# Performance work log

Measured on AMD Instinct MI355X. Metric: run time of the kernel, lower is better.

## Reference

```python
import jax, jax.numpy as jnp
import numpy as np

WS = (4, 4, 4)          # window size (D, H, W)
DIM = 96
HEADS = 8
HEAD_DIM = DIM // HEADS
SCALE = HEAD_DIM ** (-0.5)
N = WS[0] * WS[1] * WS[2]  # 64 tokens per window


def _relative_position_index(ws):
    coords = np.stack(np.meshgrid(np.arange(ws[0]), np.arange(ws[1]), np.arange(ws[2]), indexing='ij'))
    cf = coords.reshape(3, -1)                       # [3, N]
    rel = cf[:, :, None] - cf[:, None, :]            # [3, N, N]
    rel = rel.transpose(1, 2, 0).astype(np.int64)    # [N, N, 3]
    rel[:, :, 0] += ws[0] - 1
    rel[:, :, 1] += ws[1] - 1
    rel[:, :, 2] += ws[2] - 1
    rel[:, :, 0] *= (2 * ws[1] - 1) * (2 * ws[2] - 1)
    rel[:, :, 1] *= 2 * ws[2] - 1
    return jnp.asarray(rel.sum(-1))                  # [N, N]

REL_IDX = _relative_position_index(WS)


def setup_inputs() -> dict:
    key = jax.random.key(0)
    ks = jax.random.split(key, 6)
    B = 4096   # total windows (64 images x 64 windows)
    nW = 64
    table_size = (2 * WS[0] - 1) * (2 * WS[1] - 1) * (2 * WS[2] - 1)  # 343
    return {
        'x': jax.random.normal(ks[0], (B, N, DIM), jnp.float32),
        'mask': jax.random.normal(ks[1], (nW, N, N), jnp.float32),
        'qkv_w': jax.random.normal(ks[2], (3 * DIM, DIM), jnp.float32) * 0.02,
        'proj_w': jax.random.normal(ks[3], (DIM, DIM), jnp.float32) * 0.02,
        'proj_b': jnp.zeros((DIM,), jnp.float32),
        'bias_table': jax.random.normal(ks[4], (table_size, HEADS), jnp.float32) * 0.02,
    }


def reference(x, mask, qkv_w, proj_w, proj_b, bias_table):
    B, n, C = x.shape
    # QKV projection (torch Linear: y = x @ W.T), split into heads
    qkv = (x @ qkv_w.T).reshape(B, n, 3, HEADS, HEAD_DIM)
    qkv = jnp.transpose(qkv, (2, 0, 3, 1, 4))        # [3, B, H, N, hd]
    q, k, v = qkv[0], qkv[1], qkv[2]
    attn = jnp.einsum('bhnd,bhmd->bhnm', q, k) * SCALE
    # gathered relative position bias: [N, N, H] -> [H, N, N]
    bias = bias_table[REL_IDX[:n, :n].reshape(-1)].reshape(n, n, HEADS)
    attn = attn + jnp.transpose(bias, (2, 0, 1))[None]
    # shifted-window mask add
    nW = mask.shape[0]
    attn = attn.reshape(B // nW, nW, HEADS, n, n) + mask[None, :, None]
    attn = attn.reshape(B, HEADS, n, n)
    attn = jax.nn.softmax(attn, axis=-1)
    out = jnp.einsum('bhnm,bhmd->bnhd', attn, v).reshape(B, n, C)
    return out @ proj_w.T + proj_b
```

## Files before the change

kernel.cpp:

```cpp
#include <hip/hip_runtime.h>
#include <hip/hip_bf16.h>
#include <stdint.h>


typedef float  f32x4  __attribute__((ext_vector_type(4)));
typedef float  f32x16 __attribute__((ext_vector_type(16)));
typedef short  short8 __attribute__((ext_vector_type(8)));

#define WS_WQKV_OFF   (8388608)
#define WS_WPROJT_OFF (8388608 + 55296)
#define LOG2E 1.4426950408889634f

__device__ __forceinline__ unsigned short f2bf(float f) {
  __hip_bfloat16 h = __float2bfloat16(f);
  return *reinterpret_cast<unsigned short*>(&h);
}
__device__ __forceinline__ uint32_t pack2(float a, float b) {
  __hip_bfloat162 h = __float22bfloat162_rn(float2{a, b});
  return *reinterpret_cast<uint32_t*>(&h);
}

__global__ void prep_weights(const float* __restrict__ qkv_w,
                             const float* __restrict__ proj_w,
                             unsigned short* __restrict__ ws16) {
  int tid = blockIdx.x * 256 + threadIdx.x;
  if (tid < 27648) {
    float v = qkv_w[tid];
    if (tid < 9216) v *= (0.28867513459481288f * LOG2E);
    ws16[WS_WQKV_OFF / 2 + tid] = f2bf(v);
  } else {
    int t = tid - 27648;
    int h = t / 1536, rem = t - h * 1536;
    int o = rem >> 4, c = rem & 15;
    float v = (c < 12) ? proj_w[o * 96 + h * 12 + c] : 0.f;
    ws16[WS_WPROJT_OFF / 2 + t] = f2bf(v);
  }
}

__global__ void prep_biasm(const float* __restrict__ mask,
                           const float* __restrict__ bias_table,
                           float* __restrict__ biasm) {
  int tid = blockIdx.x * 256 + threadIdx.x;
  int m = tid & 63;
  int r = (tid >> 6) & 63;
  int h = (tid >> 12) & 7;
  int w = tid >> 15;
  int dr = r >> 4, hr = (r >> 2) & 3, wr = r & 3;
  int dm = m >> 4, hm = (m >> 2) & 3, wm = m & 3;
  int idx = (dr - dm + 3) * 49 + (hr - hm + 3) * 7 + (wr - wm + 3);
  biasm[tid] = (bias_table[idx * 8 + h] + mask[(w * 64 + r) * 64 + m]) * LOG2E;
}

__global__ __launch_bounds__(512, 4) void attn_main(
    const float* __restrict__ x, const float* __restrict__ proj_b,
    const unsigned short* __restrict__ ws16, const float* __restrict__ biasm,
    float* __restrict__ out) {
  __shared__ __align__(16) unsigned short q_s[8][64][16];
  __shared__ __align__(16) unsigned short k_s[8][64][16];
  __shared__ __align__(16) unsigned short v_s[8][16][72];

  const int tid  = threadIdx.x;
  const int wv   = tid >> 6;
  const int lane = tid & 63;
  const int lo4 = lane & 15, hi4 = lane >> 4;
  const int lo5 = lane & 31, hi5 = lane >> 5;
  const int blk = blockIdx.x;
  const int wmask = blk & 63;

  const unsigned short* wqkv   = ws16 + WS_WQKV_OFF / 2;
  const unsigned short* wprojT = ws16 + WS_WPROJT_OFF / 2;

  const int sub = wv & 3;
  const int par = wv >> 2;
  const int trow = sub * 16 + lo4;
  const float* xrow = x + (size_t)blk * 6144 + (size_t)trow * 96;
  float4 xa[6];
#pragma unroll
  for (int ks = 0; ks < 3; ++ks) {
    xa[2 * ks]     = *(const float4*)&xrow[ks * 32 + hi4 * 8];
    xa[2 * ks + 1] = *(const float4*)&xrow[ks * 32 + hi4 * 8 + 4];
  }

  {
    int h = tid >> 6, r = tid & 63;
    *(uint2*)&q_s[h][r][12] = make_uint2(0u, 0u);
    *(uint2*)&k_s[h][r][12] = make_uint2(0u, 0u);
  }

  {
    short8 bfX[3];
#pragma unroll
    for (int ks = 0; ks < 3; ++ks) {
      union { uint32_t u[4]; short8 s; } t;
      t.u[0] = pack2(xa[2 * ks].x,     xa[2 * ks].y);
      t.u[1] = pack2(xa[2 * ks].z,     xa[2 * ks].w);
      t.u[2] = pack2(xa[2 * ks + 1].x, xa[2 * ks + 1].y);
      t.u[3] = pack2(xa[2 * ks + 1].z, xa[2 * ks + 1].w);
      bfX[ks] = t.s;
    }
    f32x4 acc[9];
#pragma unroll
    for (int i = 0; i < 9; ++i) acc[i] = (f32x4){0.f, 0.f, 0.f, 0.f};
#pragma unroll
    for (int ks = 0; ks < 3; ++ks) {
#pragma unroll
      for (int i = 0; i < 9; ++i) {
        const int mt = 2 * i + par;
        short8 afW = *(const short8*)&wqkv[(mt * 16 + lo4) * 96 + ks * 32 + hi4 * 8];
        acc[i] = __builtin_amdgcn_mfma_f32_16x16x32_bf16(afW, bfX[ks], acc[i], 0, 0, 0);
      }
    }
#pragma unroll
    for (int i = 0; i < 9; ++i) {
      const int mt = 2 * i + par;
      const int o0 = mt * 16 + hi4 * 4;
      if (o0 < 192) {
        const int sec = (o0 >= 96) ? 96 : 0;
        const int o = o0 - sec;
        const int head = o / 12, ch = o - head * 12;
        uint2 w2;
        w2.x = pack2(acc[i][0], acc[i][1]);
        w2.y = pack2(acc[i][2], acc[i][3]);
        if (sec == 0) *(uint2*)&q_s[head][trow][ch] = w2;
        else          *(uint2*)&k_s[head][trow][ch] = w2;
      } else {
        const int o = o0 - 192;
        const int head = o / 12, ch = o - head * 12;
#pragma unroll
        for (int j = 0; j < 4; ++j)
          v_s[head][ch + j][trow] = f2bf(acc[i][j]);
      }
    }
  }

  f32x16 c[2][2];
  {
    const float* bm = biasm + (size_t)(wmask * 8 + wv) * 4096;
#pragma unroll
    for (int ti = 0; ti < 2; ++ti)
#pragma unroll
      for (int tj = 0; tj < 2; ++tj)
#pragma unroll
        for (int q4 = 0; q4 < 4; ++q4) {
          float4 b4 = *(const float4*)&bm[(tj * 32 + lo5) * 64 + ti * 32 + 8 * q4 + 4 * hi5];
          c[ti][tj][4 * q4 + 0] = b4.x;
          c[ti][tj][4 * q4 + 1] = b4.y;
          c[ti][tj][4 * q4 + 2] = b4.z;
          c[ti][tj][4 * q4 + 3] = b4.w;
        }
  }
  __syncthreads();

  f32x16 oD[2];
  {
    const int h = wv;
    __builtin_amdgcn_s_setprio(1);
#pragma unroll
    for (int ti = 0; ti < 2; ++ti) {
      short8 af = *(const short8*)&k_s[h][ti * 32 + lo5][hi5 * 8];
#pragma unroll
      for (int tj = 0; tj < 2; ++tj) {
        short8 bf = *(const short8*)&q_s[h][tj * 32 + lo5][hi5 * 8];
        c[ti][tj] = __builtin_amdgcn_mfma_f32_32x32x16_bf16(af, bf, c[ti][tj], 0, 0, 0);
      }
    }
    __builtin_amdgcn_s_setprio(0);

#pragma unroll
    for (int tj = 0; tj < 2; ++tj) {
      float mx = -1e30f;
#pragma unroll
      for (int ti = 0; ti < 2; ++ti)
#pragma unroll
        for (int reg = 0; reg < 16; ++reg) mx = fmaxf(mx, c[ti][tj][reg]);
      mx = fmaxf(mx, __shfl_xor(mx, 32));
      float sum = 0.f;
#pragma unroll
      for (int ti = 0; ti < 2; ++ti)
#pragma unroll
        for (int reg = 0; reg < 16; ++reg) {
          float e = exp2f(c[ti][tj][reg] - mx);
          c[ti][tj][reg] = e;
          sum += e;
        }
      sum += __shfl_xor(sum, 32);
      float rs = 1.0f / sum;
#pragma unroll
      for (int ti = 0; ti < 2; ++ti)
#pragma unroll
        for (int reg = 0; reg < 16; ++reg) c[ti][tj][reg] *= rs;
    }

    uint32_t pkp[2][2][8];
#pragma unroll
    for (int ti = 0; ti < 2; ++ti)
#pragma unroll
      for (int tj = 0; tj < 2; ++tj)
#pragma unroll
        for (int u = 0; u < 8; ++u)
          pkp[ti][tj][u] = pack2(c[ti][tj][2 * u], c[ti][tj][2 * u + 1]);

    oD[0] = (f32x16)(0.f); oD[1] = (f32x16)(0.f);
#pragma unroll
    for (int kc = 0; kc < 4; ++kc) {
      const int ti = kc >> 1, base = 4 * (kc & 1);
      short8 av = *(const short8*)&v_s[h][lo5 & 15][kc * 16 + hi5 * 8];
#pragma unroll
      for (int tj = 0; tj < 2; ++tj) {
        uint32_t A0 = pkp[ti][tj][base + 0], A1 = pkp[ti][tj][base + 1];
        uint32_t A2 = pkp[ti][tj][base + 2], A3 = pkp[ti][tj][base + 3];
        uint32_t k0 = hi5 ? A2 : A0, k1 = hi5 ? A3 : A1;
        uint32_t s0 = (uint32_t)__shfl_xor((int)(hi5 ? A0 : A2), 32);
        uint32_t s1 = (uint32_t)__shfl_xor((int)(hi5 ? A1 : A3), 32);
        union { uint32_t u[4]; short8 s; } bfr;
        bfr.u[0] = hi5 ? s0 : k0;
        bfr.u[1] = hi5 ? s1 : k1;
        bfr.u[2] = hi5 ? k0 : s0;
        bfr.u[3] = hi5 ? k1 : s1;
        __builtin_amdgcn_s_setprio(1);
        oD[tj] = __builtin_amdgcn_mfma_f32_32x32x16_bf16(av, bfr.s, oD[tj], 0, 0, 0);
        __builtin_amdgcn_s_setprio(0);
      }
    }

#pragma unroll
    for (int tj = 0; tj < 2; ++tj) {
      const int q = tj * 32 + lo5;
      uint2 w2;
      w2.x = pack2(oD[tj][0], oD[tj][1]);
      w2.y = pack2(oD[tj][2], oD[tj][3]);
      *(uint2*)&q_s[h][q][4 * hi5] = w2;
      if (hi5 == 0) {
        uint2 w3;
        w3.x = pack2(oD[tj][4], oD[tj][5]);
        w3.y = pack2(oD[tj][6], oD[tj][7]);
        *(uint2*)&q_s[h][q][8] = w3;
      }
    }
  }
  __syncthreads();

  {
    const int mt = wv >> 1;
    const int nb = (wv & 1) * 3;
    const int arow = mt * 16 + lo4;
    const int hh   = hi4 >> 1;
    const int off8 = (hi4 & 1) * 8;
    f32x4 acc[3];
#pragma unroll
    for (int nt = 0; nt < 3; ++nt) acc[nt] = (f32x4){0.f, 0.f, 0.f, 0.f};
#pragma unroll
    for (int ks = 0; ks < 4; ++ks) {
      const int hsel = ks * 2 + hh;
      short8 af = *(const short8*)&q_s[hsel][arow][off8];
#pragma unroll
      for (int nt = 0; nt < 3; ++nt) {
        const int ntg = nb + nt;
        short8 bf = *(const short8*)&wprojT[((size_t)hsel * 96 + ntg * 16 + lo4) * 16 + off8];
        acc[nt] = __builtin_amdgcn_mfma_f32_16x16x32_bf16(af, bf, acc[nt], 0, 0, 0);
      }
    }
    float* od = out + (size_t)blk * (64 * 96);
#pragma unroll
    for (int nt = 0; nt < 3; ++nt) {
      const int ntg = nb + nt;
      float pb = proj_b[ntg * 16 + lo4];
#pragma unroll
      for (int j = 0; j < 4; ++j)
        od[(mt * 16 + hi4 * 4 + j) * 96 + ntg * 16 + lo4] = acc[nt][j] + pb;
    }
  }
}

extern "C" void kernel_launch(void* const* d_in, const int* in_sizes, int n_in,
                              void* d_out, int out_size, void* d_ws, size_t ws_size,
                              hipStream_t stream) {
  const float* x          = (const float*)d_in[0];
  const float* mask       = (const float*)d_in[1];
  const float* qkv_w      = (const float*)d_in[2];
  const float* proj_w     = (const float*)d_in[3];
  const float* proj_b     = (const float*)d_in[4];
  const float* bias_table = (const float*)d_in[5];

  float* biasm = (float*)d_ws;
  unsigned short* ws16 = (unsigned short*)d_ws;

  prep_weights<<<156, 256, 0, stream>>>(qkv_w, proj_w, ws16);
  prep_biasm<<<8192, 256, 0, stream>>>(mask, bias_table, biasm);
  attn_main<<<4096, 512, 0, stream>>>(x, proj_b, ws16, biasm, (float*)d_out);
}
```

Measured before the change: 177.0 us.

## Make attention kernel persistent over eight windows with prefetch of next input

The main kernel now launches 512 blocks, and each block loops over 8 windows spaced 512 apart, so the window-mask index (blk & 63) stays the same across iterations. It prefetches the next window's x rows into registers while the current window's attention runs, and loads the projection weight fragments into registers before the output projection. The aim is to cut block launch overhead and hide global load latency. In exchange it adds a barrier per iteration and raises register pressure, and 512 blocks may underfill the GPU.

Measured after the change: 493.2 us. 179% more time.

```diff
diff --git a/kernel.cpp b/kernel.cpp
--- a/kernel.cpp
+++ b/kernel.cpp
@@ -70,24 +70,34 @@
   const unsigned short* wqkv   = ws16 + WS_WQKV_OFF / 2;
   const unsigned short* wprojT = ws16 + WS_WPROJT_OFF / 2;
 
-  const int sub = wv & 3;
-  const int par = wv >> 2;
-  const int trow = sub * 16 + lo4;
-  const float* xrow = x + (size_t)blk * 6144 + (size_t)trow * 96;
-  float4 xa[6];
-#pragma unroll
-  for (int ks = 0; ks < 3; ++ks) {
-    xa[2 * ks]     = *(const float4*)&xrow[ks * 32 + hi4 * 8];
-    xa[2 * ks + 1] = *(const float4*)&xrow[ks * 32 + hi4 * 8 + 4];
-  }
-
   {
     int h = tid >> 6, r = tid & 63;
     *(uint2*)&q_s[h][r][12] = make_uint2(0u, 0u);
     *(uint2*)&k_s[h][r][12] = make_uint2(0u, 0u);
   }
 
+  const int sub = wv & 3;
+  const int par = wv >> 2;
+  const int trow = sub * 16 + lo4;
+  const int mt3 = wv >> 1;
+  const int nb3 = (wv & 1) * 3;
+  const int arow3 = mt3 * 16 + lo4;
+  const int hh3 = hi4 >> 1;
+  const int off8 = (hi4 & 1) * 8;
+
+  float4 xa[6];
   {
+    const float* xrow = x + (size_t)blk * 6144 + (size_t)trow * 96;
+#pragma unroll
+    for (int ks = 0; ks < 3; ++ks) {
+      xa[2 * ks]     = *(const float4*)&xrow[ks * 32 + hi4 * 8];
+      xa[2 * ks + 1] = *(const float4*)&xrow[ks * 32 + hi4 * 8 + 4];
+    }
+  }
+
+  for (int it = 0; it < 8; ++it) {
+    const int win = (it << 9) | blk;
+
     short8 bfX[3];
 #pragma unroll
     for (int ks = 0; ks < 3; ++ks) {
@@ -98,177 +108,192 @@
       t.u[3] = pack2(xa[2 * ks + 1].z, xa[2 * ks + 1].w);
       bfX[ks] = t.s;
     }
-    f32x4 acc[9];
-#pragma unroll
-    for (int i = 0; i < 9; ++i) acc[i] = (f32x4){0.f, 0.f, 0.f, 0.f};
-#pragma unroll
-    for (int ks = 0; ks < 3; ++ks) {
+
+    {
+      f32x4 acc[9];
+#pragma unroll
+      for (int i = 0; i < 9; ++i) acc[i] = (f32x4){0.f, 0.f, 0.f, 0.f};
+#pragma unroll
+      for (int ks = 0; ks < 3; ++ks) {
+#pragma unroll
+        for (int i = 0; i < 9; ++i) {
+          const int mt = 2 * i + par;
+          short8 afW = *(const short8*)&wqkv[(mt * 16 + lo4) * 96 + ks * 32 + hi4 * 8];
+          acc[i] = __builtin_amdgcn_mfma_f32_16x16x32_bf16(afW, bfX[ks], acc[i], 0, 0, 0);
+        }
+      }
 #pragma unroll
       for (int i = 0; i < 9; ++i) {
         const int mt = 2 * i + par;
-        short8 afW = *(const short8*)&wqkv[(mt * 16 + lo4) * 96 + ks * 32 + hi4 * 8];
-        acc[i] = __builtin_amdgcn_mfma_f32_16x16x32_bf16(afW, bfX[ks], acc[i], 0, 0, 0);
-      }
-    }
-#pragma unroll
-    for (int i = 0; i < 9; ++i) {
-      const int mt = 2 * i + par;
-      const int o0 = mt * 16 + hi4 * 4;
-      if (o0 < 192) {
-        const int sec = (o0 >= 96) ? 96 : 0;
-        const int o = o0 - sec;
-        const int head = o / 12, ch = o - head * 12;
+        const int o0 = mt * 16 + hi4 * 4;
+        if (o0 < 192) {
+          const int sec = (o0 >= 96) ? 96 : 0;
+          const int o = o0 - sec;
+          const int head = o / 12, ch = o - head * 12;
+          uint2 w2;
+          w2.x = pack2(acc[i][0], acc[i][1]);
+          w2.y = pack2(acc[i][2], acc[i][3]);
+          if (sec == 0) *(uint2*)&q_s[head][trow][ch] = w2;
+          else          *(uint2*)&k_s[head][trow][ch] = w2;
+        } else {
+          const int o = o0 - 192;
+          const int head = o / 12, ch = o - head * 12;
+#pragma unroll
+          for (int j = 0; j < 4; ++j)
+            v_s[head][ch + j][trow] = f2bf(acc[i][j]);
+        }
+      }
+    }
+
+    if (it < 7) {
+      const float* xrow = x + (size_t)(win + 512) * 6144 + (size_t)trow * 96;
+#pragma unroll
+      for (int ks = 0; ks < 3; ++ks) {
+        xa[2 * ks]     = *(const float4*)&xrow[ks * 32 + hi4 * 8];
+        xa[2 * ks + 1] = *(const float4*)&xrow[ks * 32 + hi4 * 8 + 4];
+      }
+    }
+
+    f32x16 c[2][2];
+    {
+      const float* bm = biasm + (size_t)(wmask * 8 + wv) * 4096;
+#pragma unroll
+      for (int ti = 0; ti < 2; ++ti)
+#pragma unroll
+        for (int tj = 0; tj < 2; ++tj)
+#pragma unroll
+          for (int q4 = 0; q4 < 4; ++q4) {
+            float4 b4 = *(const float4*)&bm[(tj * 32 + lo5) * 64 + ti * 32 + 8 * q4 + 4 * hi5];
+            c[ti][tj][4 * q4 + 0] = b4.x;
+            c[ti][tj][4 * q4 + 1] = b4.y;
+            c[ti][tj][4 * q4 + 2] = b4.z;
+            c[ti][tj][4 * q4 + 3] = b4.w;
+          }
+    }
+    __syncthreads();
+
+    f32x16 oD[2];
+    {
+      const int h = wv;
+      __builtin_amdgcn_s_setprio(1);
+#pragma unroll
+      for (int ti = 0; ti < 2; ++ti) {
+        short8 af = *(const short8*)&k_s[h][ti * 32 + lo5][hi5 * 8];
+#pragma unroll
+        for (int tj = 0; tj < 2; ++tj) {
+          short8 bf = *(const short8*)&q_s[h][tj * 32 + lo5][hi5 * 8];
+          c[ti][tj] = __builtin_amdgcn_mfma_f32_32x32x16_bf16(af, bf, c[ti][tj], 0, 0, 0);
+        }
+      }
+      __builtin_amdgcn_s_setprio(0);
+
+#pragma unroll
+      for (int tj = 0; tj < 2; ++tj) {
+        float mx = -1e30f;
+#pragma unroll
+        for (int ti = 0; ti < 2; ++ti)
+#pragma unroll
+          for (int reg = 0; reg < 16; ++reg) mx = fmaxf(mx, c[ti][tj][reg]);
+        mx = fmaxf(mx, __shfl_xor(mx, 32));
+        float sum = 0.f;
+#pragma unroll
+        for (int ti = 0; ti < 2; ++ti)
+#pragma unroll
+          for (int reg = 0; reg < 16; ++reg) {
+            float e = exp2f(c[ti][tj][reg] - mx);
+            c[ti][tj][reg] = e;
+            sum += e;
+          }
+        sum += __shfl_xor(sum, 32);
+        float rs = 1.0f / sum;
+#pragma unroll
+        for (int ti = 0; ti < 2; ++ti)
+#pragma unroll
+          for (int reg = 0; reg < 16; ++reg) c[ti][tj][reg] *= rs;
+      }
+
+      uint32_t pkp[2][2][8];
+#pragma unroll
+      for (int ti = 0; ti < 2; ++ti)
+#pragma unroll
+        for (int tj = 0; tj < 2; ++tj)
+#pragma unroll
+          for (int u = 0; u < 8; ++u)
+            pkp[ti][tj][u] = pack2(c[ti][tj][2 * u], c[ti][tj][2 * u + 1]);
+
+      oD[0] = (f32x16)(0.f); oD[1] = (f32x16)(0.f);
+#pragma unroll
+      for (int kc = 0; kc < 4; ++kc) {
+        const int ti = kc >> 1, base = 4 * (kc & 1);
+        short8 av = *(const short8*)&v_s[h][lo5 & 15][kc * 16 + hi5 * 8];
+#pragma unroll
+        for (int tj = 0; tj < 2; ++tj) {
+          uint32_t A0 = pkp[ti][tj][base + 0], A1 = pkp[ti][tj][base + 1];
+          uint32_t A2 = pkp[ti][tj][base + 2], A3 = pkp[ti][tj][base + 3];
+          uint32_t k0 = hi5 ? A2 : A0, k1 = hi5 ? A3 : A1;
+          uint32_t s0 = (uint32_t)__shfl_xor((int)(hi5 ? A0 : A2), 32);
+          uint32_t s1 = (uint32_t)__shfl_xor((int)(hi5 ? A1 : A3), 32);
+          union { uint32_t u[4]; short8 s; } bfr;
+          bfr.u[0] = hi5 ? s0 : k0;
+          bfr.u[1] = hi5 ? s1 : k1;
+          bfr.u[2] = hi5 ? k0 : s0;
+          bfr.u[3] = hi5 ? k1 : s1;
+          __builtin_amdgcn_s_setprio(1);
+          oD[tj] = __builtin_amdgcn_mfma_f32_32x32x16_bf16(av, bfr.s, oD[tj], 0, 0, 0);
+          __builtin_amdgcn_s_setprio(0);
+        }
+      }
+    }
+
+    short8 wf[12];
+#pragma unroll
+    for (int ks = 0; ks < 4; ++ks)
+#pragma unroll
+      for (int nt = 0; nt < 3; ++nt)
+        wf[ks * 3 + nt] = *(const short8*)
+            &wprojT[((size_t)(ks * 2 + hh3) * 96 + (nb3 + nt) * 16 + lo4) * 16 + off8];
+
+    {
+      const int h = wv;
+#pragma unroll
+      for (int tj = 0; tj < 2; ++tj) {
+        const int q = tj * 32 + lo5;
         uint2 w2;
-        w2.x = pack2(acc[i][0], acc[i][1]);
-        w2.y = pack2(acc[i][2], acc[i][3]);
-        if (sec == 0) *(uint2*)&q_s[head][trow][ch] = w2;
-        else          *(uint2*)&k_s[head][trow][ch] = w2;
-      } else {
-        const int o = o0 - 192;
-        const int head = o / 12, ch = o - head * 12;
+        w2.x = pack2(oD[tj][0], oD[tj][1]);
+        w2.y = pack2(oD[tj][2], oD[tj][3]);
+        *(uint2*)&q_s[h][q][4 * hi5] = w2;
+        if (hi5 == 0) {
+          uint2 w3;
+          w3.x = pack2(oD[tj][4], oD[tj][5]);
+          w3.y = pack2(oD[tj][6], oD[tj][7]);
+          *(uint2*)&q_s[h][q][8] = w3;
+        }
+      }
+    }
+    __syncthreads();
+
+    {
+      f32x4 acc[3];
+#pragma unroll
+      for (int nt = 0; nt < 3; ++nt) acc[nt] = (f32x4){0.f, 0.f, 0.f, 0.f};
+#pragma unroll
+      for (int ks = 0; ks < 4; ++ks) {
+        short8 af = *(const short8*)&q_s[ks * 2 + hh3][arow3][off8];
+#pragma unroll
+        for (int nt = 0; nt < 3; ++nt)
+          acc[nt] = __builtin_amdgcn_mfma_f32_16x16x32_bf16(af, wf[ks * 3 + nt], acc[nt], 0, 0, 0);
+      }
+      float* od = out + (size_t)win * 6144;
+#pragma unroll
+      for (int nt = 0; nt < 3; ++nt) {
+        const int ntg = nb3 + nt;
+        float pb = proj_b[ntg * 16 + lo4];
 #pragma unroll
         for (int j = 0; j < 4; ++j)
-          v_s[head][ch + j][trow] = f2bf(acc[i][j]);
-      }
-    }
-  }
-
-  f32x16 c[2][2];
-  {
-    const float* bm = biasm + (size_t)(wmask * 8 + wv) * 4096;
-#pragma unroll
-    for (int ti = 0; ti < 2; ++ti)
-#pragma unroll
-      for (int tj = 0; tj < 2; ++tj)
-#pragma unroll
-        for (int q4 = 0; q4 < 4; ++q4) {
-          float4 b4 = *(const float4*)&bm[(tj * 32 + lo5) * 64 + ti * 32 + 8 * q4 + 4 * hi5];
-          c[ti][tj][4 * q4 + 0] = b4.x;
-          c[ti][tj][4 * q4 + 1] = b4.y;
-          c[ti][tj][4 * q4 + 2] = b4.z;
-          c[ti][tj][4 * q4 + 3] = b4.w;
-        }
-  }
-  __syncthreads();
-
-  f32x16 oD[2];
-  {
-    const int h = wv;
-    __builtin_amdgcn_s_setprio(1);
-#pragma unroll
-    for (int ti = 0; ti < 2; ++ti) {
-      short8 af = *(const short8*)&k_s[h][ti * 32 + lo5][hi5 * 8];
-#pragma unroll
-      for (int tj = 0; tj < 2; ++tj) {
-        short8 bf = *(const short8*)&q_s[h][tj * 32 + lo5][hi5 * 8];
-        c[ti][tj] = __builtin_amdgcn_mfma_f32_32x32x16_bf16(af, bf, c[ti][tj], 0, 0, 0);
-      }
-    }
-    __builtin_amdgcn_s_setprio(0);
-
-#pragma unroll
-    for (int tj = 0; tj < 2; ++tj) {
-      float mx = -1e30f;
-#pragma unroll
-      for (int ti = 0; ti < 2; ++ti)
-#pragma unroll
-        for (int reg = 0; reg < 16; ++reg) mx = fmaxf(mx, c[ti][tj][reg]);
-      mx = fmaxf(mx, __shfl_xor(mx, 32));
-      float sum = 0.f;
-#pragma unroll
-      for (int ti = 0; ti < 2; ++ti)
-#pragma unroll
-        for (int reg = 0; reg < 16; ++reg) {
-          float e = exp2f(c[ti][tj][reg] - mx);
-          c[ti][tj][reg] = e;
-          sum += e;
-        }
-      sum += __shfl_xor(sum, 32);
-      float rs = 1.0f / sum;
-#pragma unroll
-      for (int ti = 0; ti < 2; ++ti)
-#pragma unroll
-        for (int reg = 0; reg < 16; ++reg) c[ti][tj][reg] *= rs;
-    }
-
-    uint32_t pkp[2][2][8];
-#pragma unroll
-    for (int ti = 0; ti < 2; ++ti)
-#pragma unroll
-      for (int tj = 0; tj < 2; ++tj)
-#pragma unroll
-        for (int u = 0; u < 8; ++u)
-          pkp[ti][tj][u] = pack2(c[ti][tj][2 * u], c[ti][tj][2 * u + 1]);
-
-    oD[0] = (f32x16)(0.f); oD[1] = (f32x16)(0.f);
-#pragma unroll
-    for (int kc = 0; kc < 4; ++kc) {
-      const int ti = kc >> 1, base = 4 * (kc & 1);
-      short8 av = *(const short8*)&v_s[h][lo5 & 15][kc * 16 + hi5 * 8];
-#pragma unroll
-      for (int tj = 0; tj < 2; ++tj) {
-        uint32_t A0 = pkp[ti][tj][base + 0], A1 = pkp[ti][tj][base + 1];
-        uint32_t A2 = pkp[ti][tj][base + 2], A3 = pkp[ti][tj][base + 3];
-        uint32_t k0 = hi5 ? A2 : A0, k1 = hi5 ? A3 : A1;
-        uint32_t s0 = (uint32_t)__shfl_xor((int)(hi5 ? A0 : A2), 32);
-        uint32_t s1 = (uint32_t)__shfl_xor((int)(hi5 ? A1 : A3), 32);
-        union { uint32_t u[4]; short8 s; } bfr;
-        bfr.u[0] = hi5 ? s0 : k0;
-        bfr.u[1] = hi5 ? s1 : k1;
-        bfr.u[2] = hi5 ? k0 : s0;
-        bfr.u[3] = hi5 ? k1 : s1;
-        __builtin_amdgcn_s_setprio(1);
-        oD[tj] = __builtin_amdgcn_mfma_f32_32x32x16_bf16(av, bfr.s, oD[tj], 0, 0, 0);
-        __builtin_amdgcn_s_setprio(0);
-      }
-    }
-
-#pragma unroll
-    for (int tj = 0; tj < 2; ++tj) {
-      const int q = tj * 32 + lo5;
-      uint2 w2;
-      w2.x = pack2(oD[tj][0], oD[tj][1]);
-      w2.y = pack2(oD[tj][2], oD[tj][3]);
-      *(uint2*)&q_s[h][q][4 * hi5] = w2;
-      if (hi5 == 0) {
-        uint2 w3;
-        w3.x = pack2(oD[tj][4], oD[tj][5]);
-        w3.y = pack2(oD[tj][6], oD[tj][7]);
-        *(uint2*)&q_s[h][q][8] = w3;
-      }
-    }
-  }
-  __syncthreads();
-
-  {
-    const int mt = wv >> 1;
-    const int nb = (wv & 1) * 3;
-    const int arow = mt * 16 + lo4;
-    const int hh   = hi4 >> 1;
-    const int off8 = (hi4 & 1) * 8;
-    f32x4 acc[3];
-#pragma unroll
-    for (int nt = 0; nt < 3; ++nt) acc[nt] = (f32x4){0.f, 0.f, 0.f, 0.f};
-#pragma unroll
-    for (int ks = 0; ks < 4; ++ks) {
-      const int hsel = ks * 2 + hh;
-      short8 af = *(const short8*)&q_s[hsel][arow][off8];
-#pragma unroll
-      for (int nt = 0; nt < 3; ++nt) {
-        const int ntg = nb + nt;
-        short8 bf = *(const short8*)&wprojT[((size_t)hsel * 96 + ntg * 16 + lo4) * 16 + off8];
-        acc[nt] = __builtin_amdgcn_mfma_f32_16x16x32_bf16(af, bf, acc[nt], 0, 0, 0);
-      }
-    }
-    float* od = out + (size_t)blk * (64 * 96);
-#pragma unroll
-    for (int nt = 0; nt < 3; ++nt) {
-      const int ntg = nb + nt;
-      float pb = proj_b[ntg * 16 + lo4];
-#pragma unroll
-      for (int j = 0; j < 4; ++j)
-        od[(mt * 16 + hi4 * 4 + j) * 96 + ntg * 16 + lo4] = acc[nt][j] + pb;
-    }
+          od[(mt3 * 16 + hi4 * 4 + j) * 96 + ntg * 16 + lo4] = acc[nt][j] + pb;
+      }
+    }
+    __syncthreads();
   }
 }
 
@@ -287,5 +312,5 @@
 
   prep_weights<<<156, 256, 0, stream>>>(qkv_w, proj_w, ws16);
   prep_biasm<<<8192, 256, 0, stream>>>(mask, bias_table, biasm);
-  attn_main<<<4096, 512, 0, stream>>>(x, proj_b, ws16, biasm, (float*)d_out);
-}
+  attn_main<<<512, 512, 0, stream>>>(x, proj_b, ws16, biasm, (float*)d_out);
+}
```
